# Performance work log

Measured on AMD Instinct MI355X. Metric: run time of the kernel, lower is better.

Reference implementation:

```python
import jax, jax.numpy as jnp
import numpy as np

B, N, D = 8, 8192, 512
HID_ATT = D // 8          # input_dim // num_heads = 64
TOPK = max(1, int(N * 0.3))  # 2457


def _mlp2(x, W1, b1, W2, b2):
    # 2-layer MLP: Linear -> GELU -> Linear (inference mode: dropout/norm off)
    h = jax.nn.gelu(x @ W1 + b1)
    return h @ W2 + b2


def setup_inputs() -> dict:
    key = jax.random.key(0)
    ks = jax.random.split(key, 9)
    s = lambda k, sh, fan: jax.random.normal(k, sh, jnp.float32) * (1.0 / np.sqrt(fan))
    return {
        "x": jax.random.normal(ks[0], (B, N, D), jnp.float32),
        # attention-score MLP: D -> HID_ATT -> 1
        "aW1": s(ks[1], (D, HID_ATT), D),
        "ab1": jnp.zeros((HID_ATT,), jnp.float32),
        "aW2": s(ks[2], (HID_ATT, 1), HID_ATT),
        "ab2": jnp.zeros((1,), jnp.float32),
        # projection MLP: D -> D -> D
        "pW1": s(ks[3], (D, D), D),
        "pb1": jnp.zeros((D,), jnp.float32),
        "pW2": s(ks[4], (D, D), D),
        "pb2": jnp.zeros((D,), jnp.float32),
    }


def reference(x, aW1, ab1, aW2, ab2, pW1, pb1, pW2, pb2):
    # per-instance attention score -> sigmoid weight, [B, N]
    weights = jax.nn.sigmoid(_mlp2(x, aW1, ab1, aW2, ab2)[..., 0])
    # top-k per bag (largest)
    topk_scores, topk_idx = jax.lax.top_k(weights, TOPK)  # [B, TOPK]
    # gather selected instances, scale by score, mean over selected -> [B, D]
    sel = jnp.take_along_axis(x, topk_idx[..., None], axis=1)  # [B, TOPK, D]
    emb = jnp.mean(sel * topk_scores[..., None], axis=1)       # [B, D]
    projection = _mlp2(emb, pW1, pb1, pW2, pb2)                # [B, D]
    return projection, weights
```

## Files before the change

### kernel.cpp

```cpp
#include <hip/hip_runtime.h>
#include <math.h>

#define B_BAGS 8
#define N_INST 8192
#define D_DIM  512
#define H_ATT  64
#define TOPK_K 2457
#define ROWS_TOTAL (B_BAGS * N_INST)

typedef __attribute__((ext_vector_type(8))) short bf16x8;
typedef __attribute__((ext_vector_type(4))) float f32x4;
typedef __attribute__((ext_vector_type(4))) unsigned short u16x4;

#define WS_W1T_HI 0
#define WS_W1T_LO 65536
#define WS_META   131072
#define WS_PART3  131584
#define WS_PART1  (WS_PART3 + 8*64*512*4)
#define WS_PART2  (WS_PART1 + 8*8*512*4)

__device__ __forceinline__ unsigned short bf16_rn(float f) {
  unsigned int x = __float_as_uint(f);
  unsigned int r = (x + 0x7FFFu + ((x >> 16) & 1u)) >> 16;
  return (unsigned short)r;
}
__device__ __forceinline__ float bf16_f(unsigned short u) {
  return __uint_as_float(((unsigned int)u) << 16);
}
__device__ __forceinline__ float gelu_f(float v) {
  float u = 0.7978845608028654f * (v + 0.044715f * v * v * v);
  return 0.5f * v * (1.0f + tanhf(u));
}

__global__ __launch_bounds__(256) void k_prep(const float* __restrict__ aW1,
                                              unsigned short* __restrict__ hi,
                                              unsigned short* __restrict__ lo) {
  int o = blockIdx.x * 256 + threadIdx.x;
  if (o >= H_ATT * D_DIM) return;
  int n = o >> 9;
  int k = o & 511;
  float v = aW1[k * H_ATT + n];
  unsigned short h = bf16_rn(v);
  unsigned short l = bf16_rn(v - bf16_f(h));
  hi[o] = h;
  lo[o] = l;
}

#define BM 128
#define BK 64
#define LDK 72

__global__ __launch_bounds__(256, 2) void k_scores(
    const float* __restrict__ x,
    const unsigned short* __restrict__ w1t_hi,
    const unsigned short* __restrict__ w1t_lo,
    const float* __restrict__ ab1, const float* __restrict__ aW2,
    const float* __restrict__ ab2, float* __restrict__ wout) {
  __shared__ unsigned short A_hi[BM * LDK];
  __shared__ unsigned short A_lo[BM * LDK];
  __shared__ unsigned short Bh[H_ATT * LDK];
  __shared__ unsigned short Bl[H_ATT * LDK];

  int tid = threadIdx.x;
  int wave = tid >> 6, lane = tid & 63;
  int rowBase = blockIdx.x * BM;

  f32x4 acc[2][4];
#pragma unroll
  for (int s = 0; s < 2; s++)
#pragma unroll
    for (int t = 0; t < 4; t++) acc[s][t] = (f32x4){0.f, 0.f, 0.f, 0.f};

  float4 xa[8];
  int4 wbh[2], wbl[2];

  auto issue = [&](int kc) {
#pragma unroll
    for (int i = 0; i < 8; i++) {
      int r = (tid >> 4) + i * 16;
      int kk = (tid & 15) << 2;
      xa[i] = *reinterpret_cast<const float4*>(
          x + (size_t)(rowBase + r) * D_DIM + kc + kk);
    }
#pragma unroll
    for (int i = 0; i < 2; i++) {
      int idx = tid + i * 256;
      int n = idx >> 3;
      int kk = (idx & 7) << 3;
      wbh[i] = *reinterpret_cast<const int4*>(w1t_hi + n * D_DIM + kc + kk);
      wbl[i] = *reinterpret_cast<const int4*>(w1t_lo + n * D_DIM + kc + kk);
    }
  };
  auto cvt_store = [&]() {
#pragma unroll
    for (int i = 0; i < 8; i++) {
      const float4 v = xa[i];
      unsigned short h0 = bf16_rn(v.x), h1 = bf16_rn(v.y), h2 = bf16_rn(v.z), h3 = bf16_rn(v.w);
      unsigned short l0 = bf16_rn(v.x - bf16_f(h0));
      unsigned short l1 = bf16_rn(v.y - bf16_f(h1));
      unsigned short l2 = bf16_rn(v.z - bf16_f(h2));
      unsigned short l3 = bf16_rn(v.w - bf16_f(h3));
      int a = ((tid >> 4) + i * 16) * LDK + ((tid & 15) << 2);
      *reinterpret_cast<u16x4*>(&A_hi[a]) = (u16x4){h0, h1, h2, h3};
      *reinterpret_cast<u16x4*>(&A_lo[a]) = (u16x4){l0, l1, l2, l3};
    }
#pragma unroll
    for (int i = 0; i < 2; i++) {
      int idx = tid + i * 256;
      int n = idx >> 3;
      int kk = (idx & 7) << 3;
      *reinterpret_cast<int4*>(&Bh[n * LDK + kk]) = wbh[i];
      *reinterpret_cast<int4*>(&Bl[n * LDK + kk]) = wbl[i];
    }
  };
  auto mfma_phase = [&]() {
#pragma unroll
    for (int k2 = 0; k2 < 2; k2++) {
      int ko = k2 * 32 + (lane >> 4) * 8;
      bf16x8 afh[2], afl[2], bfh[4], bfl[4];
#pragma unroll
      for (int s = 0; s < 2; s++) {
        int r = wave * 32 + s * 16 + (lane & 15);
        afh[s] = *reinterpret_cast<const bf16x8*>(&A_hi[r * LDK + ko]);
        afl[s] = *reinterpret_cast<const bf16x8*>(&A_lo[r * LDK + ko]);
      }
#pragma unroll
      for (int t = 0; t < 4; t++) {
        int n = t * 16 + (lane & 15);
        bfh[t] = *reinterpret_cast<const bf16x8*>(&Bh[n * LDK + ko]);
        bfl[t] = *reinterpret_cast<const bf16x8*>(&Bl[n * LDK + ko]);
      }
#pragma unroll
      for (int s = 0; s < 2; s++)
#pragma unroll
        for (int t = 0; t < 4; t++) {
          acc[s][t] = __builtin_amdgcn_mfma_f32_16x16x32_bf16(afl[s], bfh[t], acc[s][t], 0, 0, 0);
          acc[s][t] = __builtin_amdgcn_mfma_f32_16x16x32_bf16(afh[s], bfl[t], acc[s][t], 0, 0, 0);
          acc[s][t] = __builtin_amdgcn_mfma_f32_16x16x32_bf16(afh[s], bfh[t], acc[s][t], 0, 0, 0);
        }
    }
  };

  issue(0);
  cvt_store();
  __syncthreads();
  for (int kc8 = 0; kc8 < 8; kc8++) {
    if (kc8 < 7) issue((kc8 + 1) * BK);
    mfma_phase();
    __syncthreads();
    if (kc8 < 7) {
      cvt_store();
      __syncthreads();
    }
  }

  int c0 = lane & 15, quad = lane >> 4;
  float w2v[4], b1v[4];
#pragma unroll
  for (int t = 0; t < 4; t++) {
    w2v[t] = aW2[t * 16 + c0];
    b1v[t] = ab1[t * 16 + c0];
  }
  float bias2 = ab2[0];
#pragma unroll
  for (int s = 0; s < 2; s++) {
    float p[4] = {0.f, 0.f, 0.f, 0.f};
#pragma unroll
    for (int t = 0; t < 4; t++)
#pragma unroll
      for (int r = 0; r < 4; r++) {
        float h = gelu_f(acc[s][t][r] + b1v[t]);
        p[r] += h * w2v[t];
      }
#pragma unroll
    for (int off = 1; off < 16; off <<= 1)
#pragma unroll
      for (int r = 0; r < 4; r++) p[r] += __shfl_xor(p[r], off, 64);
    if (c0 == 0) {
      int row = rowBase + wave * 32 + s * 16 + quad * 4;
#pragma unroll
      for (int r = 0; r < 4; r++) {
        float sc = p[r] + bias2;
        wout[row + r] = 1.0f / (1.0f + expf(-sc));
      }
    }
  }
}

__global__ __launch_bounds__(256) void k_topk(const float* __restrict__ wout,
                                              unsigned int* __restrict__ meta) {
  int b = blockIdx.x;
  const float* w = wout + b * N_INST;
  int tid = threadIdx.x;
  unsigned int v[32];
#pragma unroll
  for (int j = 0; j < 32; j++) v[j] = __float_as_uint(w[j * 256 + tid]);

  __shared__ int red[2][4];
  int lane = tid & 63, wv = tid >> 6;
  int pb = 0;

  auto blocksum = [&](int c) -> int {
#pragma unroll
    for (int off = 32; off > 0; off >>= 1) c += __shfl_down(c, off, 64);
    if (lane == 0) red[pb][wv] = c;
    __syncthreads();
    int s = red[pb][0] + red[pb][1] + red[pb][2] + red[pb][3];
    pb ^= 1;
    return s;
  };

  unsigned int lo = 0u, hi = 0x3F800001u;
  while (hi - lo > 1u) {
    unsigned int mid = lo + ((hi - lo) >> 1);
    int c = 0;
#pragma unroll
    for (int j = 0; j < 32; j++) c += (v[j] >= mid) ? 1 : 0;
    int s = blocksum(c);
    if (s >= TOPK_K) lo = mid; else hi = mid;
  }
  unsigned int T = lo;

  int c1;
  {
    int c = 0;
#pragma unroll
    for (int j = 0; j < 32; j++) c += (v[j] > T) ? 1 : 0;
    c1 = blocksum(c);
  }
  int needed = TOPK_K - c1;

  unsigned int tm = 0;
#pragma unroll
  for (int j = 0; j < 32; j++) tm |= (v[j] == T ? 1u : 0u) << j;
  int lom = -1, him = N_INST - 1;
  while (him - lom > 1) {
    int mid = (lom + him) >> 1;
    unsigned int mask = 0u;
    if (mid >= tid) {
      unsigned int jmax = (unsigned int)(mid - tid) >> 8;
      mask = (2u << jmax) - 1u;
    }
    int s = blocksum((int)__popc(tm & mask));
    if (s >= needed) him = mid; else lom = mid;
  }
  if (tid == 0) {
    meta[b] = T;
    ((int*)meta)[8 + b] = him;
  }
}

__global__ __launch_bounds__(256) void k_gather(const float* __restrict__ x,
                                                const float* __restrict__ wout,
                                                const unsigned int* __restrict__ meta,
                                                float* __restrict__ part3) {
  int b = blockIdx.x >> 6;
  int blk = blockIdx.x & 63;
  unsigned int T = meta[b];
  int Icut = ((const int*)meta)[8 + b];
  int tid = threadIdx.x;

  __shared__ int idxs[128];
  __shared__ float wgts[128];
  __shared__ int wcnt[2];

  int r = blk * 128 + tid;
  bool sel = false;
  float wvv = 0.f;
  int pos = 0;
  if (tid < 128) {
    wvv = wout[b * N_INST + r];
    unsigned int wu = __float_as_uint(wvv);
    sel = (wu > T) || (wu == T && r <= Icut);
    unsigned long long m = __ballot(sel);
    int lane = tid & 63;
    pos = __popcll(m & ((1ull << lane) - 1ull));
    if (lane == 0) wcnt[tid >> 6] = __popcll(m);
  }
  __syncthreads();
  int total = wcnt[0] + wcnt[1];
  if (sel) {
    int base = (tid >= 64) ? wcnt[0] : 0;
    idxs[base + pos] = r;
    wgts[base + pos] = wvv;
  }
  __syncthreads();

  float2 acc = {0.f, 0.f};
  const float* xb = x + (size_t)b * N_INST * D_DIM;
#pragma unroll 8
  for (int i = 0; i < total; i++) {
    int rr = idxs[i];
    float ww = wgts[i];
    const float2 xv = *reinterpret_cast<const float2*>(xb + (size_t)rr * D_DIM + tid * 2);
    acc.x += ww * xv.x;
    acc.y += ww * xv.y;
  }
  *reinterpret_cast<float2*>(part3 + (size_t)(b * 64 + blk) * D_DIM + tid * 2) = acc;
}

__global__ __launch_bounds__(256) void k_proj1(const float* __restrict__ part3,
                                               const float* __restrict__ pW1,
                                               float* __restrict__ part1) {
  int jt = blockIdx.x & 7, kt = blockIdx.x >> 3;
  __shared__ float emb_s[512];
  int tid = threadIdx.x;
#pragma unroll
  for (int h = 0; h < 2; h++) {
    int vi = tid + h * 256;
    int b = vi >> 6, d0 = vi & 63;
    const float* p = part3 + (size_t)b * 64 * 512 + kt * 64 + d0;
    float e = 0.f;
#pragma unroll 8
    for (int j = 0; j < 64; j++) e += p[j * 512];
    emb_s[vi] = e * (1.0f / TOPK_K);
  }
  __syncthreads();
  int col = tid & 63, bg = tid >> 6;
  float a0 = 0.f, a1 = 0.f;
  const float* wrow = pW1 + (size_t)(kt * 64) * 512 + jt * 64 + col;
#pragma unroll 8
  for (int q = 0; q < 64; q++) {
    float wq = wrow[q * 512];
    a0 += emb_s[(bg * 2) * 64 + q] * wq;
    a1 += emb_s[(bg * 2 + 1) * 64 + q] * wq;
  }
  part1[kt * 4096 + (bg * 2) * 512 + jt * 64 + col] = a0;
  part1[kt * 4096 + (bg * 2 + 1) * 512 + jt * 64 + col] = a1;
}

__global__ __launch_bounds__(256) void k_proj2(const float* __restrict__ part1,
                                               const float* __restrict__ pb1,
                                               const float* __restrict__ pW2,
                                               float* __restrict__ part2) {
  int jt = blockIdx.x & 7, kt = blockIdx.x >> 3;
  __shared__ float h_s[512];
  int tid = threadIdx.x;
#pragma unroll
  for (int h = 0; h < 2; h++) {
    int vi = tid + h * 256;
    int b = vi >> 6, j0 = vi & 63;
    int jj = kt * 64 + j0;
    float s = pb1[jj];
#pragma unroll
    for (int p = 0; p < 8; p++) s += part1[p * 4096 + b * 512 + jj];
    h_s[vi] = gelu_f(s);
  }
  __syncthreads();
  int col = tid & 63, bg = tid >> 6;
  float a0 = 0.f, a1 = 0.f;
  const float* wrow = pW2 + (size_t)(kt * 64) * 512 + jt * 64 + col;
#pragma unroll 8
  for (int q = 0; q < 64; q++) {
    float wq = wrow[q * 512];
    a0 += h_s[(bg * 2) * 64 + q] * wq;
    a1 += h_s[(bg * 2 + 1) * 64 + q] * wq;
  }
  part2[kt * 4096 + (bg * 2) * 512 + jt * 64 + col] = a0;
  part2[kt * 4096 + (bg * 2 + 1) * 512 + jt * 64 + col] = a1;
}

__global__ __launch_bounds__(512) void k_proj3(const float* __restrict__ part2,
                                               const float* __restrict__ pb2,
                                               float* __restrict__ out) {
  int o = blockIdx.x * 512 + threadIdx.x;
  int bj = o & 511;
  float s = pb2[bj];
#pragma unroll
  for (int p = 0; p < 8; p++) s += part2[p * 4096 + o];
  out[o] = s;
}

extern "C" void kernel_launch(void* const* d_in, const int* in_sizes, int n_in,
                              void* d_out, int out_size, void* d_ws, size_t ws_size,
                              hipStream_t stream) {
  (void)in_sizes; (void)n_in; (void)out_size; (void)ws_size;
  const float* x   = (const float*)d_in[0];
  const float* aW1 = (const float*)d_in[1];
  const float* ab1 = (const float*)d_in[2];
  const float* aW2 = (const float*)d_in[3];
  const float* ab2 = (const float*)d_in[4];
  const float* pW1 = (const float*)d_in[5];
  const float* pb1 = (const float*)d_in[6];
  const float* pW2 = (const float*)d_in[7];
  const float* pb2 = (const float*)d_in[8];

  float* out  = (float*)d_out;
  float* wout = out + B_BAGS * D_DIM;

  char* ws = (char*)d_ws;
  unsigned short* w1t_hi = (unsigned short*)(ws + WS_W1T_HI);
  unsigned short* w1t_lo = (unsigned short*)(ws + WS_W1T_LO);
  unsigned int*   meta   = (unsigned int*)(ws + WS_META);
  float* part3 = (float*)(ws + WS_PART3);
  float* part1 = (float*)(ws + WS_PART1);
  float* part2 = (float*)(ws + WS_PART2);

  k_prep<<<dim3((H_ATT * D_DIM + 255) / 256), dim3(256), 0, stream>>>(aW1, w1t_hi, w1t_lo);
  k_scores<<<dim3(ROWS_TOTAL / BM), dim3(256), 0, stream>>>(x, w1t_hi, w1t_lo, ab1, aW2, ab2, wout);
  k_topk<<<dim3(B_BAGS), dim3(256), 0, stream>>>(wout, meta);
  k_gather<<<dim3(B_BAGS * 64), dim3(256), 0, stream>>>(x, wout, meta, part3);
  k_proj1<<<dim3(64), dim3(256), 0, stream>>>(part3, pW1, part1);
  k_proj2<<<dim3(64), dim3(256), 0, stream>>>(part1, pb1, pW2, part2);
  k_proj3<<<dim3(B_BAGS), dim3(512), 0, stream>>>(part2, pb2, out);
}
```

Baseline: 266.5 us.

## Load MFMA fragments straight from global memory, dropping LDS staging in score GEMM

```diff
diff --git a/kernel.cpp b/kernel.cpp
--- a/kernel.cpp
+++ b/kernel.cpp
@@ -10,7 +10,6 @@
 
 typedef __attribute__((ext_vector_type(8))) short bf16x8;
 typedef __attribute__((ext_vector_type(4))) float f32x4;
-typedef __attribute__((ext_vector_type(4))) unsigned short u16x4;
 
 #define WS_W1T_HI 0
 #define WS_W1T_LO 65536
@@ -30,6 +29,19 @@
 __device__ __forceinline__ float gelu_f(float v) {
   float u = 0.7978845608028654f * (v + 0.044715f * v * v * v);
   return 0.5f * v * (1.0f + tanhf(u));
+}
+
+__device__ __forceinline__ void cvt_hilo(const float4 u, const float4 v,
+                                         bf16x8& h, bf16x8& l) {
+  float f[8] = {u.x, u.y, u.z, u.w, v.x, v.y, v.z, v.w};
+#pragma unroll
+  for (int i = 0; i < 8; i++) {
+    unsigned int b = __float_as_uint(f[i]);
+    unsigned int hb = b & 0xFFFF0000u;
+    float r = f[i] - __uint_as_float(hb);
+    h[i] = (short)(b >> 16);
+    l[i] = (short)(__float_as_uint(r) >> 16);
+  }
 }
 
 __global__ __launch_bounds__(256) void k_prep(const float* __restrict__ aW1,
@@ -47,114 +59,69 @@
 }
 
 #define BM 128
-#define BK 64
-#define LDK 72
-
-__global__ __launch_bounds__(256, 2) void k_scores(
+
+__global__ __launch_bounds__(256) void k_scores(
     const float* __restrict__ x,
     const unsigned short* __restrict__ w1t_hi,
     const unsigned short* __restrict__ w1t_lo,
     const float* __restrict__ ab1, const float* __restrict__ aW2,
     const float* __restrict__ ab2, float* __restrict__ wout) {
-  __shared__ unsigned short A_hi[BM * LDK];
-  __shared__ unsigned short A_lo[BM * LDK];
-  __shared__ unsigned short Bh[H_ATT * LDK];
-  __shared__ unsigned short Bl[H_ATT * LDK];
-
   int tid = threadIdx.x;
   int wave = tid >> 6, lane = tid & 63;
+  int c0 = lane & 15, quad = lane >> 4;
   int rowBase = blockIdx.x * BM;
 
+  const float* xr[2];
+  xr[0] = x + (size_t)(rowBase + wave * 32 + c0) * D_DIM;
+  xr[1] = xr[0] + 16 * D_DIM;
+  const int kq = quad * 8;
+
   f32x4 acc[2][4];
 #pragma unroll
   for (int s = 0; s < 2; s++)
 #pragma unroll
     for (int t = 0; t < 4; t++) acc[s][t] = (f32x4){0.f, 0.f, 0.f, 0.f};
 
-  float4 xa[8];
-  int4 wbh[2], wbl[2];
-
-  auto issue = [&](int kc) {
-#pragma unroll
-    for (int i = 0; i < 8; i++) {
-      int r = (tid >> 4) + i * 16;
-      int kk = (tid & 15) << 2;
-      xa[i] = *reinterpret_cast<const float4*>(
-          x + (size_t)(rowBase + r) * D_DIM + kc + kk);
+  const unsigned short* bh0 = w1t_hi + c0 * D_DIM + kq;
+  const unsigned short* bl0 = w1t_lo + c0 * D_DIM + kq;
+
+  float4 a0[2], a1[2], n0[2], n1[2];
+#pragma unroll
+  for (int s = 0; s < 2; s++) {
+    a0[s] = *reinterpret_cast<const float4*>(xr[s] + kq);
+    a1[s] = *reinterpret_cast<const float4*>(xr[s] + kq + 4);
+  }
+
+  for (int ks = 0; ks < 16; ks++) {
+    if (ks < 15) {
+      int kb = (ks + 1) * 32 + kq;
+#pragma unroll
+      for (int s = 0; s < 2; s++) {
+        n0[s] = *reinterpret_cast<const float4*>(xr[s] + kb);
+        n1[s] = *reinterpret_cast<const float4*>(xr[s] + kb + 4);
+      }
     }
-#pragma unroll
-    for (int i = 0; i < 2; i++) {
-      int idx = tid + i * 256;
-      int n = idx >> 3;
-      int kk = (idx & 7) << 3;
-      wbh[i] = *reinterpret_cast<const int4*>(w1t_hi + n * D_DIM + kc + kk);
-      wbl[i] = *reinterpret_cast<const int4*>(w1t_lo + n * D_DIM + kc + kk);
+    bf16x8 bfh[4], bfl[4];
+#pragma unroll
+    for (int t = 0; t < 4; t++) {
+      bfh[t] = *reinterpret_cast<const bf16x8*>(bh0 + t * 16 * D_DIM + ks * 32);
+      bfl[t] = *reinterpret_cast<const bf16x8*>(bl0 + t * 16 * D_DIM + ks * 32);
     }
-  };
-  auto cvt_store = [&]() {
-#pragma unroll
-    for (int i = 0; i < 8; i++) {
-      const float4 v = xa[i];
-      unsigned short h0 = bf16_rn(v.x), h1 = bf16_rn(v.y), h2 = bf16_rn(v.z), h3 = bf16_rn(v.w);
-      unsigned short l0 = bf16_rn(v.x - bf16_f(h0));
-      unsigned short l1 = bf16_rn(v.y - bf16_f(h1));
-      unsigned short l2 = bf16_rn(v.z - bf16_f(h2));
-      unsigned short l3 = bf16_rn(v.w - bf16_f(h3));
-      int a = ((tid >> 4) + i * 16) * LDK + ((tid & 15) << 2);
-      *reinterpret_cast<u16x4*>(&A_hi[a]) = (u16x4){h0, h1, h2, h3};
-      *reinterpret_cast<u16x4*>(&A_lo[a]) = (u16x4){l0, l1, l2, l3};
-    }
-#pragma unroll
-    for (int i = 0; i < 2; i++) {
-      int idx = tid + i * 256;
-      int n = idx >> 3;
-      int kk = (idx & 7) << 3;
-      *reinterpret_cast<int4*>(&Bh[n * LDK + kk]) = wbh[i];
-      *reinterpret_cast<int4*>(&Bl[n * LDK + kk]) = wbl[i];
-    }
-  };
-  auto mfma_phase = [&]() {
-#pragma unroll
-    for (int k2 = 0; k2 < 2; k2++) {
-      int ko = k2 * 32 + (lane >> 4) * 8;
-      bf16x8 afh[2], afl[2], bfh[4], bfl[4];
-#pragma unroll
-      for (int s = 0; s < 2; s++) {
-        int r = wave * 32 + s * 16 + (lane & 15);
-        afh[s] = *reinterpret_cast<const bf16x8*>(&A_hi[r * LDK + ko]);
-        afl[s] = *reinterpret_cast<const bf16x8*>(&A_lo[r * LDK + ko]);
+    bf16x8 afh[2], afl[2];
+#pragma unroll
+    for (int s = 0; s < 2; s++) cvt_hilo(a0[s], a1[s], afh[s], afl[s]);
+#pragma unroll
+    for (int s = 0; s < 2; s++)
+#pragma unroll
+      for (int t = 0; t < 4; t++) {
+        acc[s][t] = __builtin_amdgcn_mfma_f32_16x16x32_bf16(afl[s], bfh[t], acc[s][t], 0, 0, 0);
+        acc[s][t] = __builtin_amdgcn_mfma_f32_16x16x32_bf16(afh[s], bfl[t], acc[s][t], 0, 0, 0);
+        acc[s][t] = __builtin_amdgcn_mfma_f32_16x16x32_bf16(afh[s], bfh[t], acc[s][t], 0, 0, 0);
       }
 #pragma unroll
-      for (int t = 0; t < 4; t++) {
-        int n = t * 16 + (lane & 15);
-        bfh[t] = *reinterpret_cast<const bf16x8*>(&Bh[n * LDK + ko]);
-        bfl[t] = *reinterpret_cast<const bf16x8*>(&Bl[n * LDK + ko]);
-      }
-#pragma unroll
-      for (int s = 0; s < 2; s++)
-#pragma unroll
-        for (int t = 0; t < 4; t++) {
-          acc[s][t] = __builtin_amdgcn_mfma_f32_16x16x32_bf16(afl[s], bfh[t], acc[s][t], 0, 0, 0);
-          acc[s][t] = __builtin_amdgcn_mfma_f32_16x16x32_bf16(afh[s], bfl[t], acc[s][t], 0, 0, 0);
-          acc[s][t] = __builtin_amdgcn_mfma_f32_16x16x32_bf16(afh[s], bfh[t], acc[s][t], 0, 0, 0);
-        }
-    }
-  };
-
-  issue(0);
-  cvt_store();
-  __syncthreads();
-  for (int kc8 = 0; kc8 < 8; kc8++) {
-    if (kc8 < 7) issue((kc8 + 1) * BK);
-    mfma_phase();
-    __syncthreads();
-    if (kc8 < 7) {
-      cvt_store();
-      __syncthreads();
-    }
-  }
-
-  int c0 = lane & 15, quad = lane >> 4;
+    for (int s = 0; s < 2; s++) { a0[s] = n0[s]; a1[s] = n1[s]; }
+  }
+
   float w2v[4], b1v[4];
 #pragma unroll
   for (int t = 0; t < 4; t++) {
```

After: 273.4 us. 2.6% more time.

## Fuse top-k into scores tail block, fold proj3 into proj2, widen gather loads

Applied to the files above, without the earlier changes.

```diff
diff --git a/kernel.cpp b/kernel.cpp
--- a/kernel.cpp
+++ b/kernel.cpp
@@ -34,7 +34,9 @@
 
 __global__ __launch_bounds__(256) void k_prep(const float* __restrict__ aW1,
                                               unsigned short* __restrict__ hi,
-                                              unsigned short* __restrict__ lo) {
+                                              unsigned short* __restrict__ lo,
+                                              unsigned int* __restrict__ counters) {
+  if (blockIdx.x == 0 && threadIdx.x < 4) counters[threadIdx.x] = 0u;
   int o = blockIdx.x * 256 + threadIdx.x;
   if (o >= H_ATT * D_DIM) return;
   int n = o >> 9;
@@ -55,11 +57,13 @@
     const unsigned short* __restrict__ w1t_hi,
     const unsigned short* __restrict__ w1t_lo,
     const float* __restrict__ ab1, const float* __restrict__ aW2,
-    const float* __restrict__ ab2, float* __restrict__ wout) {
+    const float* __restrict__ ab2, float* __restrict__ wout,
+    unsigned int* __restrict__ meta, unsigned int* __restrict__ counters) {
   __shared__ unsigned short A_hi[BM * LDK];
   __shared__ unsigned short A_lo[BM * LDK];
   __shared__ unsigned short Bh[H_ATT * LDK];
   __shared__ unsigned short Bl[H_ATT * LDK];
+  __shared__ unsigned int rank_s;
 
   int tid = threadIdx.x;
   int wave = tid >> 6, lane = tid & 63;
@@ -185,68 +189,69 @@
       }
     }
   }
-}
-
-__global__ __launch_bounds__(256) void k_topk(const float* __restrict__ wout,
-                                              unsigned int* __restrict__ meta) {
-  int b = blockIdx.x;
-  const float* w = wout + b * N_INST;
-  int tid = threadIdx.x;
-  unsigned int v[32];
-#pragma unroll
-  for (int j = 0; j < 32; j++) v[j] = __float_as_uint(w[j * 256 + tid]);
-
-  __shared__ int red[2][4];
-  int lane = tid & 63, wv = tid >> 6;
-  int pb = 0;
-
-  auto blocksum = [&](int c) -> int {
-#pragma unroll
-    for (int off = 32; off > 0; off >>= 1) c += __shfl_down(c, off, 64);
-    if (lane == 0) red[pb][wv] = c;
-    __syncthreads();
-    int s = red[pb][0] + red[pb][1] + red[pb][2] + red[pb][3];
-    pb ^= 1;
-    return s;
-  };
-
-  unsigned int lo = 0u, hi = 0x3F800001u;
-  while (hi - lo > 1u) {
-    unsigned int mid = lo + ((hi - lo) >> 1);
-    int c = 0;
-#pragma unroll
-    for (int j = 0; j < 32; j++) c += (v[j] >= mid) ? 1 : 0;
-    int s = blocksum(c);
-    if (s >= TOPK_K) lo = mid; else hi = mid;
-  }
-  unsigned int T = lo;
-
-  int c1;
-  {
-    int c = 0;
-#pragma unroll
-    for (int j = 0; j < 32; j++) c += (v[j] > T) ? 1 : 0;
-    c1 = blocksum(c);
-  }
-  int needed = TOPK_K - c1;
-
-  unsigned int tm = 0;
-#pragma unroll
-  for (int j = 0; j < 32; j++) tm |= (v[j] == T ? 1u : 0u) << j;
-  int lom = -1, him = N_INST - 1;
-  while (him - lom > 1) {
-    int mid = (lom + him) >> 1;
-    unsigned int mask = 0u;
-    if (mid >= tid) {
-      unsigned int jmax = (unsigned int)(mid - tid) >> 8;
-      mask = (2u << jmax) - 1u;
-    }
-    int s = blocksum((int)__popc(tm & mask));
-    if (s >= needed) him = mid; else lom = mid;
-  }
-  if (tid == 0) {
-    meta[b] = T;
-    ((int*)meta)[8 + b] = him;
+
+  __threadfence();
+  __syncthreads();
+  if (tid == 0) rank_s = atomicAdd(&counters[0], 1u);
+  __syncthreads();
+  if (rank_s != (unsigned int)(gridDim.x - 1)) return;
+  __threadfence();
+
+  for (int bb = wave; bb < B_BAGS; bb += 4) {
+    const float* w = wout + bb * N_INST;
+    unsigned int v[128];
+#pragma unroll
+    for (int j = 0; j < 128; j++) v[j] = __float_as_uint(w[j * 64 + lane]);
+
+    auto wsum = [&](int c) -> int {
+#pragma unroll
+      for (int off = 1; off < 64; off <<= 1) c += __shfl_xor(c, off, 64);
+      return c;
+    };
+
+    unsigned int lo = 0u, hi = 0x3F800001u;
+    while (hi - lo > 1u) {
+      unsigned int mid = lo + ((hi - lo) >> 1);
+      int c = 0;
+#pragma unroll
+      for (int j = 0; j < 128; j++) c += (v[j] >= mid) ? 1 : 0;
+      if (wsum(c) >= TOPK_K) lo = mid; else hi = mid;
+    }
+    unsigned int T = lo;
+
+    int c1 = 0;
+#pragma unroll
+    for (int j = 0; j < 128; j++) c1 += (v[j] > T) ? 1 : 0;
+    c1 = wsum(c1);
+    int needed = TOPK_K - c1;
+
+    unsigned long long tm0 = 0ull, tm1 = 0ull;
+#pragma unroll
+    for (int j = 0; j < 64; j++) tm0 |= (v[j] == T ? 1ull : 0ull) << j;
+#pragma unroll
+    for (int j = 0; j < 64; j++) tm1 |= (v[64 + j] == T ? 1ull : 0ull) << j;
+
+    int lom = -1, him = N_INST - 1;
+    while (him - lom > 1) {
+      int mid = (lom + him) >> 1;
+      int c = 0;
+      if (mid >= lane) {
+        unsigned int jmax = (unsigned int)(mid - lane) >> 6;
+        unsigned int j0 = jmax > 63u ? 63u : jmax;
+        unsigned long long m0 = (2ull << j0) - 1ull;
+        unsigned long long m1 = 0ull;
+        if (jmax >= 64u) {
+          unsigned int j1 = (jmax - 64u) > 63u ? 63u : (jmax - 64u);
+          m1 = (2ull << j1) - 1ull;
+        }
+        c = __popcll(tm0 & m0) + __popcll(tm1 & m1);
+      }
+      if (wsum(c) >= needed) him = mid; else lom = mid;
+    }
+    if (lane == 0) {
+      meta[bb] = T;
+      ((int*)meta)[8 + bb] = him;
+    }
   }
 }
 
@@ -263,6 +268,7 @@
   __shared__ int idxs[128];
   __shared__ float wgts[128];
   __shared__ int wcnt[2];
+  __shared__ float4 xfer[128];
 
   int r = blk * 128 + tid;
   bool sel = false;
@@ -286,17 +292,31 @@
   }
   __syncthreads();
 
-  float2 acc = {0.f, 0.f};
+  int half = tid >> 7;
+  int L = tid & 127;
+  float4 acc = {0.f, 0.f, 0.f, 0.f};
   const float* xb = x + (size_t)b * N_INST * D_DIM;
-#pragma unroll 8
-  for (int i = 0; i < total; i++) {
-    int rr = idxs[i];
-    float ww = wgts[i];
-    const float2 xv = *reinterpret_cast<const float2*>(xb + (size_t)rr * D_DIM + tid * 2);
-    acc.x += ww * xv.x;
-    acc.y += ww * xv.y;
-  }
-  *reinterpret_cast<float2*>(part3 + (size_t)(b * 64 + blk) * D_DIM + tid * 2) = acc;
+  int i2 = total & ~1;
+#pragma unroll 4
+  for (int i = 0; i < i2; i += 2) {
+    int rr = idxs[i + half];
+    float ww = wgts[i + half];
+    const float4 xv = *reinterpret_cast<const float4*>(xb + (size_t)rr * D_DIM + L * 4);
+    acc.x += ww * xv.x; acc.y += ww * xv.y; acc.z += ww * xv.z; acc.w += ww * xv.w;
+  }
+  if ((total & 1) && half == 0) {
+    int rr = idxs[i2];
+    float ww = wgts[i2];
+    const float4 xv = *reinterpret_cast<const float4*>(xb + (size_t)rr * D_DIM + L * 4);
+    acc.x += ww * xv.x; acc.y += ww * xv.y; acc.z += ww * xv.z; acc.w += ww * xv.w;
+  }
+  if (half == 1) xfer[L] = acc;
+  __syncthreads();
+  if (half == 0) {
+    float4 o = xfer[L];
+    acc.x += o.x; acc.y += o.y; acc.z += o.z; acc.w += o.w;
+    *reinterpret_cast<float4*>(part3 + (size_t)(b * 64 + blk) * D_DIM + L * 4) = acc;
+  }
 }
 
 __global__ __launch_bounds__(256) void k_proj1(const float* __restrict__ part3,
@@ -332,9 +352,13 @@
 __global__ __launch_bounds__(256) void k_proj2(const float* __restrict__ part1,
                                                const float* __restrict__ pb1,
                                                const float* __restrict__ pW2,
-                                               float* __restrict__ part2) {
+                                               float* __restrict__ part2,
+                                               const float* __restrict__ pb2,
+                                               float* __restrict__ out,
+                                               unsigned int* __restrict__ counters) {
   int jt = blockIdx.x & 7, kt = blockIdx.x >> 3;
   __shared__ float h_s[512];
+  __shared__ unsigned int rank_s;
   int tid = threadIdx.x;
 #pragma unroll
   for (int h = 0; h < 2; h++) {
@@ -358,17 +382,19 @@
   }
   part2[kt * 4096 + (bg * 2) * 512 + jt * 64 + col] = a0;
   part2[kt * 4096 + (bg * 2 + 1) * 512 + jt * 64 + col] = a1;
-}
-
-__global__ __launch_bounds__(512) void k_proj3(const float* __restrict__ part2,
-                                               const float* __restrict__ pb2,
-                                               float* __restrict__ out) {
-  int o = blockIdx.x * 512 + threadIdx.x;
-  int bj = o & 511;
-  float s = pb2[bj];
-#pragma unroll
-  for (int p = 0; p < 8; p++) s += part2[p * 4096 + o];
-  out[o] = s;
+
+  __threadfence();
+  __syncthreads();
+  if (tid == 0) rank_s = atomicAdd(&counters[1], 1u);
+  __syncthreads();
+  if (rank_s != (unsigned int)(gridDim.x - 1)) return;
+  __threadfence();
+  for (int oo = tid; oo < 4096; oo += 256) {
+    float s = pb2[oo & 511];
+#pragma unroll
+    for (int p = 0; p < 8; p++) s += part2[p * 4096 + oo];
+    out[oo] = s;
+  }
 }
 
 extern "C" void kernel_launch(void* const* d_in, const int* in_sizes, int n_in,
@@ -392,15 +418,14 @@
   unsigned short* w1t_hi = (unsigned short*)(ws + WS_W1T_HI);
   unsigned short* w1t_lo = (unsigned short*)(ws + WS_W1T_LO);
   unsigned int*   meta   = (unsigned int*)(ws + WS_META);
+  unsigned int*   counters = meta + 16;
   float* part3 = (float*)(ws + WS_PART3);
   float* part1 = (float*)(ws + WS_PART1);
   float* part2 = (float*)(ws + WS_PART2);
 
-  k_prep<<<dim3((H_ATT * D_DIM + 255) / 256), dim3(256), 0, stream>>>(aW1, w1t_hi, w1t_lo);
-  k_scores<<<dim3(ROWS_TOTAL / BM), dim3(256), 0, stream>>>(x, w1t_hi, w1t_lo, ab1, aW2, ab2, wout);
-  k_topk<<<dim3(B_BAGS), dim3(256), 0, stream>>>(wout, meta);
+  k_prep<<<dim3((H_ATT * D_DIM + 255) / 256), dim3(256), 0, stream>>>(aW1, w1t_hi, w1t_lo, counters);
+  k_scores<<<dim3(ROWS_TOTAL / BM), dim3(256), 0, stream>>>(x, w1t_hi, w1t_lo, ab1, aW2, ab2, wout, meta, counters);
   k_gather<<<dim3(B_BAGS * 64), dim3(256), 0, stream>>>(x, wout, meta, part3);
   k_proj1<<<dim3(64), dim3(256), 0, stream>>>(part3, pW1, part1);
-  k_proj2<<<dim3(64), dim3(256), 0, stream>>>(part1, pb1, pW2, part2);
-  k_proj3<<<dim3(B_BAGS), dim3(512), 0, stream>>>(part2, pb2, out);
-}
+  k_proj2<<<dim3(64), dim3(256), 0, stream>>>(part1, pb1, pW2, part2, pb2, out, counters);
+}
```

New measurement: 379.0 us. 42.2% more time.
